# Kernel optimization log

Measured on AMD Instinct MI355X. Metric: run time of the kernel, lower is better.

Reference implementation:

```python
import jax, jax.numpy as jnp
import numpy as np

N, E, F_IN, H, HID, OUT, G, NCLS = 20000, 320000, 128, 4, 64, 128, 64, 10
EPS = 1e-5
NEG_SLOPE = 0.2
# layer specs: (in_dim, heads, out_per_head, concat)
LAYERS = [(F_IN, H, HID, True), (H * HID, H, HID, True), (H * HID, 1, OUT, False)]


def setup_inputs() -> dict:
    key = jax.random.key(0)
    ks = jax.random.split(key, 24)
    s = 0.1
    inp = {
        "x": jax.random.normal(ks[0], (N, F_IN), jnp.float32),
        "edge_index": jax.random.randint(ks[1], (2, E), 0, N, jnp.int32),
        "batch": jnp.sort(jax.random.randint(ks[2], (N,), 0, G, jnp.int32)),
    }
    i = 3
    for li, (din, h, dout, concat) in enumerate(LAYERS):
        inp[f"W{li}"] = jax.random.normal(ks[i], (din, h * dout), jnp.float32) * s; i += 1
        inp[f"asrc{li}"] = jax.random.normal(ks[i], (h, dout), jnp.float32) * s; i += 1
        inp[f"adst{li}"] = jax.random.normal(ks[i], (h, dout), jnp.float32) * s; i += 1
        bdim = h * dout if concat else dout
        inp[f"b{li}"] = jnp.zeros((bdim,), jnp.float32)
        inp[f"gamma{li}"] = jnp.ones((bdim,), jnp.float32)
        inp[f"beta{li}"] = jnp.zeros((bdim,), jnp.float32)
    inp["clf_W"] = jax.random.normal(ks[i], (OUT, NCLS), jnp.float32) * s; i += 1
    inp["clf_b"] = jnp.zeros((NCLS,), jnp.float32)
    inp["dom_W1"] = jax.random.normal(ks[i], (OUT, OUT // 2), jnp.float32) * s; i += 1
    inp["dom_b1"] = jnp.zeros((OUT // 2,), jnp.float32)
    inp["dom_W2"] = jax.random.normal(ks[i], (OUT // 2, 2), jnp.float32) * s; i += 1
    inp["dom_b2"] = jnp.zeros((2,), jnp.float32)
    return inp


def _gat_layer(x, src, dst, W, a_s, a_d, b, heads, dout, concat):
    n = x.shape[0]
    h = (x @ W).reshape(n, heads, dout)                      # [N,H,D]
    es = jnp.sum(h * a_s, axis=-1)                           # [N,H]
    ed = jnp.sum(h * a_d, axis=-1)                           # [N,H]
    e = jax.nn.leaky_relu(es[src] + ed[dst], NEG_SLOPE)      # [E',H]
    m = jax.ops.segment_max(e, dst, num_segments=n)          # segment softmax over dst
    w = jnp.exp(e - m[dst])
    z = jax.ops.segment_sum(w, dst, num_segments=n)
    att = w / z[dst]                                         # [E',H]
    out = jax.ops.segment_sum(h[src] * att[:, :, None], dst, num_segments=n)  # [N,H,D]
    out = out.reshape(n, heads * dout) if concat else out.mean(axis=1)
    return out + b


def _bn(x, gamma, beta):  # training-mode BN forward (batch stats, biased var)
    mu = x.mean(axis=0)
    var = x.var(axis=0)
    return (x - mu) * jax.lax.rsqrt(var + EPS) * gamma + beta


def reference(x, edge_index, batch,
              W0, asrc0, adst0, b0, gamma0, beta0,
              W1, asrc1, adst1, b1, gamma1, beta1,
              W2, asrc2, adst2, b2, gamma2, beta2,
              clf_W, clf_b, dom_W1, dom_b1, dom_W2, dom_b2):
    n = x.shape[0]
    loop = jnp.arange(n, dtype=edge_index.dtype)
    src = jnp.concatenate([edge_index[0], loop])  # add self-loops (PyG default)
    dst = jnp.concatenate([edge_index[1], loop])
    params = [(W0, asrc0, adst0, b0, gamma0, beta0),
              (W1, asrc1, adst1, b1, gamma1, beta1),
              (W2, asrc2, adst2, b2, gamma2, beta2)]
    for (W, a_s, a_d, b, g, be), (_, heads, dout, concat) in zip(params, LAYERS):
        x = _gat_layer(x, src, dst, W, a_s, a_d, b, heads, dout, concat)
        x = jax.nn.relu(_bn(x, g, be))  # dropout disabled (inference)
    counts = jax.ops.segment_sum(jnp.ones((n,), x.dtype), batch, num_segments=G)
    feature = jax.ops.segment_sum(x, batch, num_segments=G) / jnp.maximum(counts, 1.0)[:, None]
    class_output = feature @ clf_W + clf_b
    dom_h = jax.nn.relu(feature @ dom_W1 + dom_b1)  # GRL is identity in forward
    domain_output = dom_h @ dom_W2 + dom_b2
    return (class_output, domain_output, feature)
```

## Files before the change

kernel.cpp:

```cpp
#include <hip/hip_runtime.h>
#include <hip/hip_bf16.h>

#define CAP 64
#define EPSBN 1e-5f
#define NEG_SLOPE 0.2f
#define NPARAM 24
#define POOL_SPLIT 4
#define BNB 256

typedef __attribute__((ext_vector_type(8))) short short8;
typedef __attribute__((ext_vector_type(4))) float f32x4;

static __device__ __forceinline__ float b2f(__hip_bfloat16 v) { return __bfloat162float(v); }
static __device__ __forceinline__ float u2f(unsigned short u) {
    return __uint_as_float(((unsigned int)u) << 16);
}
static __device__ __forceinline__ unsigned short f2b_rne(float f) {
    unsigned int u = __float_as_uint(f);
    u += 0x7FFF + ((u >> 16) & 1);
    return (unsigned short)(u >> 16);
}
static __device__ __forceinline__ bool is_f32(const int* flagcnt) { return *flagcnt > 32; }

__global__ void k_detect(const unsigned short* __restrict__ raw, int* flagcnt) {
    int t = threadIdx.x;
    int c = 0;
    for (int i = t; i < 4096; i += 256) {
        int e = (raw[i] >> 7) & 0xFF;
        if (e >= 200) c++;
    }
    atomicAdd(flagcnt, c);
}

struct CvtTab {
    const void* src[NPARAM];
    float* dst[NPARAM];
    int off[NPARAM + 1];
};

__global__ void k_prep(const void* __restrict__ x_in, unsigned short* __restrict__ xb16,
                       CvtTab tab,
                       unsigned short* __restrict__ Wt0, unsigned short* __restrict__ Wt1,
                       unsigned short* __restrict__ Wt2,
                       const int* flagcnt, int NX, int ptot) {
    bool f32 = is_f32(flagcnt);
    const void* W0r = tab.src[0];
    const void* W1r = tab.src[6];
    const void* W2r = tab.src[12];
    int b0 = NX, b1 = b0 + ptot, b2 = b1 + 256 * 128, b3 = b2 + 256 * 256, b4 = b3 + 128 * 256;
    for (int i = blockIdx.x * blockDim.x + threadIdx.x; i < b4; i += gridDim.x * blockDim.x) {
        if (i < b0) {
            xb16[i] = f32 ? f2b_rne(((const float*)x_in)[i]) : ((const unsigned short*)x_in)[i];
        } else if (i < b1) {
            int ii = i - b0;
            int j = 0;
            while (tab.off[j + 1] <= ii) j++;
            int k = ii - tab.off[j];
            tab.dst[j][k] = f32 ? ((const float*)tab.src[j])[k]
                                : b2f(((const __hip_bfloat16*)tab.src[j])[k]);
        } else if (i < b2) {
            int ii = i - b1;
            int f = ii >> 7, k = ii & 127;
            long src = (long)k * 256 + f;
            Wt0[ii] = f32 ? f2b_rne(((const float*)W0r)[src]) : ((const unsigned short*)W0r)[src];
        } else if (i < b3) {
            int ii = i - b2;
            int f = ii >> 8, k = ii & 255;
            long src = (long)k * 256 + f;
            Wt1[ii] = f32 ? f2b_rne(((const float*)W1r)[src]) : ((const unsigned short*)W1r)[src];
        } else {
            int ii = i - b3;
            int f = ii >> 8, k = ii & 255;
            long src = (long)k * 128 + f;
            Wt2[ii] = f32 ? f2b_rne(((const float*)W2r)[src]) : ((const unsigned short*)W2r)[src];
        }
    }
}

__global__ void k_fill_graph(const int* __restrict__ ei, int* cnt, int* adj, int E) {
    int e = blockIdx.x * blockDim.x + threadIdx.x;
    if (e < E) {
        int s = ei[e];
        int d = ei[E + e];
        int slot = atomicAdd(&cnt[d], 1);
        if (slot < CAP) adj[d * CAP + slot] = s;
    }
}

__global__ __launch_bounds__(256) void k_gemm_mfma(const unsigned short* __restrict__ A,
                                                   const unsigned short* __restrict__ Bt,
                                                   unsigned short* __restrict__ C,
                                                   const float* __restrict__ scale,
                                                   const float* __restrict__ shift,
                                                   int M, int K, int F) {
    __shared__ __align__(16) unsigned short As[64 * 40];
    __shared__ __align__(16) unsigned short Bs[64 * 40];
    int t = threadIdx.x;
    int lane = t & 63, wave = t >> 6;
    int wm = wave & 1, wf = wave >> 1;
    int m0 = blockIdx.x * 64, f0 = blockIdx.y * 64;
    int r = lane & 15, q = lane >> 4;
    int srow = t >> 2, schunk = t & 3;
    f32x4 acc[2][2] = {};
    for (int k0 = 0; k0 < K; k0 += 32) {
        uint4 av = {0, 0, 0, 0};
        int gr = m0 + srow;
        if (gr < M) {
            av = *(const uint4*)(A + (long)gr * K + k0 + schunk * 8);
            if (scale) {
                int fb = k0 + schunk * 8;
                float4 s0 = *(const float4*)(scale + fb);
                float4 s1 = *(const float4*)(scale + fb + 4);
                float4 h0 = *(const float4*)(shift + fb);
                float4 h1 = *(const float4*)(shift + fb + 4);
                unsigned short* ev = (unsigned short*)&av;
                ev[0] = f2b_rne(fmaxf(u2f(ev[0]) * s0.x + h0.x, 0.f));
                ev[1] = f2b_rne(fmaxf(u2f(ev[1]) * s0.y + h0.y, 0.f));
                ev[2] = f2b_rne(fmaxf(u2f(ev[2]) * s0.z + h0.z, 0.f));
                ev[3] = f2b_rne(fmaxf(u2f(ev[3]) * s0.w + h0.w, 0.f));
                ev[4] = f2b_rne(fmaxf(u2f(ev[4]) * s1.x + h1.x, 0.f));
                ev[5] = f2b_rne(fmaxf(u2f(ev[5]) * s1.y + h1.y, 0.f));
                ev[6] = f2b_rne(fmaxf(u2f(ev[6]) * s1.z + h1.z, 0.f));
                ev[7] = f2b_rne(fmaxf(u2f(ev[7]) * s1.w + h1.w, 0.f));
            }
        }
        *(uint4*)&As[srow * 40 + schunk * 8] = av;
        uint4 bv = *(const uint4*)(Bt + (long)(f0 + srow) * K + k0 + schunk * 8);
        *(uint4*)&Bs[srow * 40 + schunk * 8] = bv;
        __syncthreads();
        short8 a0 = *(short8*)&As[(wm * 32 + r) * 40 + q * 8];
        short8 a1 = *(short8*)&As[(wm * 32 + 16 + r) * 40 + q * 8];
        short8 b0 = *(short8*)&Bs[(wf * 32 + r) * 40 + q * 8];
        short8 b1 = *(short8*)&Bs[(wf * 32 + 16 + r) * 40 + q * 8];
        acc[0][0] = __builtin_amdgcn_mfma_f32_16x16x32_bf16(a0, b0, acc[0][0], 0, 0, 0);
        acc[0][1] = __builtin_amdgcn_mfma_f32_16x16x32_bf16(a0, b1, acc[0][1], 0, 0, 0);
        acc[1][0] = __builtin_amdgcn_mfma_f32_16x16x32_bf16(a1, b0, acc[1][0], 0, 0, 0);
        acc[1][1] = __builtin_amdgcn_mfma_f32_16x16x32_bf16(a1, b1, acc[1][1], 0, 0, 0);
        __syncthreads();
    }
    #pragma unroll
    for (int mt = 0; mt < 2; mt++) {
        #pragma unroll
        for (int reg = 0; reg < 4; reg++) {
            int row = m0 + wm * 32 + mt * 16 + q * 4 + reg;
            if (row < M) {
                C[(long)row * F + f0 + wf * 32 + r]      = f2b_rne(acc[mt][0][reg]);
                C[(long)row * F + f0 + wf * 32 + 16 + r] = f2b_rne(acc[mt][1][reg]);
            }
        }
    }
}

template <int F, int H>
__global__ __launch_bounds__(256) void k_agg(const unsigned short* __restrict__ h,
                      const int* __restrict__ cnt, const int* __restrict__ adj,
                      const float* __restrict__ a_s, const float* __restrict__ a_d,
                      const float* __restrict__ bias,
                      unsigned short* __restrict__ out, int n) {
    const int VPL = F / 64;
    const int LPH = 64 / H;
    int lane = threadIdx.x & 63;
    int dst = (blockIdx.x * blockDim.x + threadIdx.x) >> 6;
    if (dst >= n) return;
    float asv[VPL], adv[VPL];
    #pragma unroll
    for (int j = 0; j < VPL; j++) {
        asv[j] = a_s[lane * VPL + j];
        adv[j] = a_d[lane * VPL + j];
    }
    float hs[VPL];
    {
        const unsigned short* hp = h + (long)dst * F + lane * VPL;
        if (VPL == 4) {
            uint2 hv = *(const uint2*)hp;
            hs[0] = __uint_as_float(hv.x << 16); hs[1] = __uint_as_float(hv.x & 0xffff0000u);
            hs[2] = __uint_as_float(hv.y << 16); hs[3] = __uint_as_float(hv.y & 0xffff0000u);
        } else {
            unsigned int hv = *(const unsigned int*)hp;
            hs[0] = __uint_as_float(hv << 16); hs[1] = __uint_as_float(hv & 0xffff0000u);
        }
    }
    float ps = 0.f, pd = 0.f;
    #pragma unroll
    for (int j = 0; j < VPL; j++) { ps += hs[j] * asv[j]; pd += hs[j] * adv[j]; }
    #pragma unroll
    for (int m = 1; m < LPH; m <<= 1) {
        ps += __shfl_xor(ps, m, 64);
        pd += __shfl_xor(pd, m, 64);
    }
    float ed_dst = pd;
    float e = ps + ed_dst;
    e = fmaxf(e, NEG_SLOPE * e);
    float w = __expf(e);
    float z = w;
    float acc[VPL];
    #pragma unroll
    for (int j = 0; j < VPL; j++) acc[j] = w * hs[j];

    int deg = min(cnt[dst], CAP);
    const int* ap = adj + (long)dst * CAP;
    int sl = 0;
    if (deg > 0) sl = ap[lane < deg ? lane : deg - 1];
    for (int base = 0; base < deg; base += 8) {
        float hv[8][VPL];
        #pragma unroll
        for (int c = 0; c < 8; c++) {
            int idx = base + c;
            int ii = idx < deg ? idx : deg - 1;
            int s = __builtin_amdgcn_readlane(sl, ii);
            const unsigned short* hp = h + (long)s * F + lane * VPL;
            if (VPL == 4) {
                uint2 hb = *(const uint2*)hp;
                hv[c][0] = __uint_as_float(hb.x << 16);
                hv[c][1] = __uint_as_float(hb.x & 0xffff0000u);
                hv[c][2] = __uint_as_float(hb.y << 16);
                hv[c][3] = __uint_as_float(hb.y & 0xffff0000u);
            } else {
                unsigned int hb = *(const unsigned int*)hp;
                hv[c][0] = __uint_as_float(hb << 16);
                hv[c][1] = __uint_as_float(hb & 0xffff0000u);
            }
        }
        #pragma unroll
        for (int c = 0; c < 8; c++) {
            float p = 0.f;
            #pragma unroll
            for (int j = 0; j < VPL; j++) p += hv[c][j] * asv[j];
            #pragma unroll
            for (int m = 1; m < LPH; m <<= 1) p += __shfl_xor(p, m, 64);
            float ee = p + ed_dst;
            ee = fmaxf(ee, NEG_SLOPE * ee);
            float ww = __expf(ee);
            if (base + c >= deg) ww = 0.f;
            z += ww;
            #pragma unroll
            for (int j = 0; j < VPL; j++) acc[j] += ww * hv[c][j];
        }
    }
    float invz = 1.f / z;
    unsigned short pk[VPL];
    #pragma unroll
    for (int j = 0; j < VPL; j++)
        pk[j] = f2b_rne(acc[j] * invz + bias[lane * VPL + j]);
    if (VPL == 4) *(ushort4*)(out + (long)dst * F + lane * 4) = *(ushort4*)pk;
    else          *(ushort2*)(out + (long)dst * F + lane * 2) = *(ushort2*)pk;
}

template <int F>
__global__ __launch_bounds__(256) void k_bnpart(const unsigned short* __restrict__ x,
                                                float* __restrict__ partial, int n) {
    const int TPR = F / 8;
    const int RPI = 256 / TPR;
    __shared__ float sm[256 * 17];
    int t = threadIdx.x;
    int fr = t % TPR;
    int rp = t / TPR;
    int f0 = fr * 8;
    float s[8] = {}, q[8] = {};
    for (int r = blockIdx.x * RPI + rp; r < n; r += gridDim.x * RPI) {
        uint4 v = *(const uint4*)(x + (long)r * F + f0);
        const unsigned short* ev = (const unsigned short*)&v;
        #pragma unroll
        for (int j = 0; j < 8; j++) {
            float f = u2f(ev[j]);
            s[j] += f; q[j] += f * f;
        }
    }
    #pragma unroll
    for (int j = 0; j < 8; j++) { sm[t * 17 + j] = s[j]; sm[t * 17 + 8 + j] = q[j]; }
    __syncthreads();
    if (rp == 0) {
        float a[8], b[8];
        #pragma unroll
        for (int j = 0; j < 8; j++) { a[j] = sm[fr * 17 + j]; b[j] = sm[fr * 17 + 8 + j]; }
        for (int p = 1; p < RPI; p++) {
            int o = (p * TPR + fr) * 17;
            #pragma unroll
            for (int j = 0; j < 8; j++) { a[j] += sm[o + j]; b[j] += sm[o + 8 + j]; }
        }
        float* dp = partial + (long)blockIdx.x * 2 * F;
        #pragma unroll
        for (int j = 0; j < 8; j++) { dp[f0 + j] = a[j]; dp[F + f0 + j] = b[j]; }
    }
}

__global__ __launch_bounds__(64) void k_bnfold(const float* __restrict__ partial,
                         const float* __restrict__ gamma, const float* __restrict__ beta,
                         float* __restrict__ scale, float* __restrict__ shift,
                         float invN, int F, int nb) {
    int f = blockIdx.x;
    int l = threadIdx.x;
    float s = 0.f, q = 0.f;
    for (int b = l; b < nb; b += 64) {
        s += partial[(long)b * 2 * F + f];
        q += partial[(long)b * 2 * F + F + f];
    }
    #pragma unroll
    for (int m = 1; m < 64; m <<= 1) {
        s += __shfl_xor(s, m, 64);
        q += __shfl_xor(q, m, 64);
    }
    if (l == 0) {
        float mu = s * invN;
        float var = q * invN - mu * mu;
        float sc = gamma[f] * rsqrtf(var + EPSBN);
        scale[f] = sc;
        shift[f] = beta[f] - mu * sc;
    }
}

static __device__ __forceinline__ int lower_bound_i(const int* __restrict__ a, int n, int v) {
    int lo = 0, hi = n;
    while (lo < hi) { int mid = (lo + hi) >> 1; if (a[mid] < v) lo = mid + 1; else hi = mid; }
    return lo;
}

__global__ __launch_bounds__(256) void k_pool2(const unsigned short* __restrict__ x,
                                               const int* __restrict__ batch,
                                               const float* __restrict__ scale,
                                               const float* __restrict__ shift,
                                               float* __restrict__ featsum,
                                               int* __restrict__ gcnt, int n) {
    const int TPR = 32;
    const int RPI = 8;
    __shared__ float sm[256 * 5];
    int g = blockIdx.x / POOL_SPLIT;
    int part = blockIdx.x % POOL_SPLIT;
    int t = threadIdx.x;
    int fr = t % TPR;
    int rp = t / TPR;
    int f0 = fr * 4;
    int lo = lower_bound_i(batch, n, g);
    int hi = lower_bound_i(batch, n, g + 1);
    float4 sc = *(const float4*)(scale + f0);
    float4 sh = *(const float4*)(shift + f0);
    float a0 = 0.f, a1 = 0.f, a2 = 0.f, a3 = 0.f;
    for (int r = lo + part * RPI + rp; r < hi; r += POOL_SPLIT * RPI) {
        uint2 v = *(const uint2*)(x + (long)r * 128 + f0);
        a0 += fmaxf(u2f((unsigned short)(v.x & 0xffff)) * sc.x + sh.x, 0.f);
        a1 += fmaxf(u2f((unsigned short)(v.x >> 16))    * sc.y + sh.y, 0.f);
        a2 += fmaxf(u2f((unsigned short)(v.y & 0xffff)) * sc.z + sh.z, 0.f);
        a3 += fmaxf(u2f((unsigned short)(v.y >> 16))    * sc.w + sh.w, 0.f);
    }
    sm[t * 5 + 0] = a0; sm[t * 5 + 1] = a1; sm[t * 5 + 2] = a2; sm[t * 5 + 3] = a3;
    __syncthreads();
    if (rp == 0) {
        float b[4];
        #pragma unroll
        for (int j = 0; j < 4; j++) b[j] = sm[fr * 5 + j];
        for (int p = 1; p < RPI; p++)
            #pragma unroll
            for (int j = 0; j < 4; j++) b[j] += sm[(p * TPR + fr) * 5 + j];
        #pragma unroll
        for (int j = 0; j < 4; j++) atomicAdd(&featsum[g * 128 + f0 + j], b[j]);
    }
    if (t == 0 && part == 0) gcnt[g] = hi - lo;
}

__global__ void k_head(const float* __restrict__ featsum, const int* __restrict__ gcnt,
                       const float* __restrict__ clfW, const float* __restrict__ clfb,
                       const float* __restrict__ dW1, const float* __restrict__ db1,
                       const float* __restrict__ dW2, const float* __restrict__ db2,
                       void* __restrict__ out, const int* flagcnt, int G) {
    __shared__ float feat[128];
    __shared__ float dh[64];
    bool f32o = is_f32(flagcnt);
    float* of = (float*)out;
    __hip_bfloat16* ob = (__hip_bfloat16*)out;
    int g = blockIdx.x, t = threadIdx.x;
    float c = fmaxf((float)gcnt[g], 1.f);
    float fv = featsum[g * 128 + t] / c;
    feat[t] = fv;
    int fidx = G * 10 + G * 2 + g * 128 + t;
    if (f32o) of[fidx] = fv; else ob[fidx] = __float2bfloat16(fv);
    __syncthreads();
    if (t < 10) {
        float a = clfb[t];
        for (int k = 0; k < 128; k++) a += feat[k] * clfW[k * 10 + t];
        int idx = g * 10 + t;
        if (f32o) of[idx] = a; else ob[idx] = __float2bfloat16(a);
    }
    if (t < 64) {
        float a = db1[t];
        for (int k = 0; k < 128; k++) a += feat[k] * dW1[k * 64 + t];
        dh[t] = a > 0.f ? a : 0.f;
    }
    __syncthreads();
    if (t < 2) {
        float a = db2[t];
        for (int k = 0; k < 64; k++) a += dh[k] * dW2[k * 2 + t];
        int idx = G * 10 + g * 2 + t;
        if (f32o) of[idx] = a; else ob[idx] = __float2bfloat16(a);
    }
}

extern "C" void kernel_launch(void* const* d_in, const int* in_sizes, int n_in,
                              void* d_out, int out_size, void* d_ws, size_t ws_size,
                              hipStream_t stream) {
    const void* x_in = d_in[0];
    const int* ei    = (const int*)d_in[1];
    const int* batch = (const int*)d_in[2];
    const int N = in_sizes[2];
    const int E = in_sizes[1] / 2;
    const int G = 64;

    char* ws = (char*)d_ws;
    size_t off = 0;
    auto alloc = [&](size_t bytes) {
        void* p = ws + off;
        off += (bytes + 255) & ~(size_t)255;
        return p;
    };

    size_t zstart = off;
    int*   flagcnt   = (int*)alloc(256);
    float* featsum   = (float*)alloc((size_t)G * 128 * 4 + (size_t)G * 4);
    int*   gcnt      = (int*)(featsum + G * 128);
    int*   cnt       = (int*)alloc((size_t)N * 4);
    size_t zbytes = off - zstart;

    int*   adj     = (int*)alloc((size_t)N * CAP * 4);
    unsigned short* xbuf16 = (unsigned short*)alloc((size_t)N * 256 * 2);
    unsigned short* hbuf   = (unsigned short*)alloc((size_t)N * 256 * 2);
    unsigned short* xb16   = (unsigned short*)alloc((size_t)N * 256 * 2);
    unsigned short* Wt0    = (unsigned short*)alloc((size_t)256 * 128 * 2);
    unsigned short* Wt1    = (unsigned short*)alloc((size_t)256 * 256 * 2);
    unsigned short* Wt2    = (unsigned short*)alloc((size_t)128 * 256 * 2);
    float* bnpart  = (float*)alloc((size_t)BNB * 512 * 4);
    float* bnscale = (float*)alloc(3 * 512 * 4);

    float* sc0 = bnscale,        *sh0 = bnscale + 256;
    float* sc1 = bnscale + 512,  *sh1 = bnscale + 768;
    float* sc2 = bnscale + 1024, *sh2 = bnscale + 1280;

    CvtTab tab;
    float* pp[NPARAM];
    int ptot = 0;
    for (int j = 0; j < NPARAM; j++) {
        int cnt_j = in_sizes[3 + j];
        pp[j] = (float*)alloc((size_t)cnt_j * 4);
        tab.src[j] = d_in[3 + j];
        tab.dst[j] = pp[j];
        tab.off[j] = ptot;
        ptot += cnt_j;
    }
    tab.off[NPARAM] = ptot;
    float *asf0 = pp[1], *adf0 = pp[2], *bf0 = pp[3], *gf0 = pp[4], *bef0 = pp[5];
    float *asf1 = pp[7], *adf1 = pp[8], *bf1 = pp[9], *gf1 = pp[10], *bef1 = pp[11];
    float *asf2 = pp[13], *adf2 = pp[14], *bf2 = pp[15], *gf2 = pp[16], *bef2 = pp[17];
    float *clfWf = pp[18], *clfbf = pp[19], *dW1f = pp[20], *db1f = pp[21], *dW2f = pp[22], *db2f = pp[23];

    const int TPB = 256;
    int wgrid = (N + 3) / 4;
    int mblocks = (N + 63) / 64;
    float invN = 1.f / (float)N;

    hipMemsetAsync(ws + zstart, 0, zbytes, stream);
    k_detect<<<1, 256, 0, stream>>>((const unsigned short*)x_in, flagcnt);
    k_prep<<<2048, TPB, 0, stream>>>(x_in, xb16, tab, Wt0, Wt1, Wt2, flagcnt, N * 128, ptot);
    k_fill_graph<<<(E + TPB - 1) / TPB, TPB, 0, stream>>>(ei, cnt, adj, E);

    k_gemm_mfma<<<dim3(mblocks, 4), 256, 0, stream>>>(xb16, Wt0, hbuf, nullptr, nullptr, N, 128, 256);
    k_agg<256, 4><<<wgrid, 256, 0, stream>>>(hbuf, cnt, adj, asf0, adf0, bf0, xbuf16, N);
    k_bnpart<256><<<BNB, 256, 0, stream>>>(xbuf16, bnpart, N);
    k_bnfold<<<256, 64, 0, stream>>>(bnpart, gf0, bef0, sc0, sh0, invN, 256, BNB);

    k_gemm_mfma<<<dim3(mblocks, 4), 256, 0, stream>>>(xbuf16, Wt1, hbuf, sc0, sh0, N, 256, 256);
    k_agg<256, 4><<<wgrid, 256, 0, stream>>>(hbuf, cnt, adj, asf1, adf1, bf1, xbuf16, N);
    k_bnpart<256><<<BNB, 256, 0, stream>>>(xbuf16, bnpart, N);
    k_bnfold<<<256, 64, 0, stream>>>(bnpart, gf1, bef1, sc1, sh1, invN, 256, BNB);

    k_gemm_mfma<<<dim3(mblocks, 2), 256, 0, stream>>>(xbuf16, Wt2, hbuf, sc1, sh1, N, 256, 128);
    k_agg<128, 1><<<wgrid, 256, 0, stream>>>(hbuf, cnt, adj, asf2, adf2, bf2, xbuf16, N);
    k_bnpart<128><<<BNB, 256, 0, stream>>>(xbuf16, bnpart, N);
    k_bnfold<<<128, 64, 0, stream>>>(bnpart, gf2, bef2, sc2, sh2, invN, 128, BNB);

    k_pool2<<<G * POOL_SPLIT, 256, 0, stream>>>(xbuf16, batch, sc2, sh2, featsum, gcnt, N);
    k_head<<<G, 128, 0, stream>>>(featsum, gcnt, clfWf, clfbf, dW1f, db1f, dW2f, db2f,
                                  d_out, flagcnt, G);
}
```

Baseline: 316.3 us.

## Fuse BatchNorm partial statistics into aggregation and enlarge GEMM M-tile

The aggregation kernel now handles 8 destination nodes per wave and accumulates per-feature sum and sum-of-squares of its bf16 outputs. It reduces them across waves in shared memory and writes per-block partials, which removes the separate k_bnpart pass that re-read the full activation buffer. The GEMM tile grows from 64 to 128 rows per block, so each wave issues 8 MFMAs per k-step and each loaded B tile is reused more. LDS padding is also dropped (stride 40 to 32), which may add bank conflicts, and k_bnfold now reduces far more partial blocks (about 625 instead of 256).

Result: slower. 360.6 us (+14.0%).

```diff
diff --git a/kernel.cpp b/kernel.cpp
--- a/kernel.cpp
+++ b/kernel.cpp
@@ -6,7 +6,7 @@
 #define NEG_SLOPE 0.2f
 #define NPARAM 24
 #define POOL_SPLIT 4
-#define BNB 256
+#define DPW 8
 
 typedef __attribute__((ext_vector_type(8))) short short8;
 typedef __attribute__((ext_vector_type(4))) float f32x4;
@@ -93,59 +93,69 @@
                                                    const float* __restrict__ scale,
                                                    const float* __restrict__ shift,
                                                    int M, int K, int F) {
-    __shared__ __align__(16) unsigned short As[64 * 40];
-    __shared__ __align__(16) unsigned short Bs[64 * 40];
+    __shared__ __align__(16) unsigned short As[128 * 32];
+    __shared__ __align__(16) unsigned short Bs[64 * 32];
     int t = threadIdx.x;
     int lane = t & 63, wave = t >> 6;
     int wm = wave & 1, wf = wave >> 1;
-    int m0 = blockIdx.x * 64, f0 = blockIdx.y * 64;
+    int m0 = blockIdx.x * 128, f0 = blockIdx.y * 64;
     int r = lane & 15, q = lane >> 4;
-    int srow = t >> 2, schunk = t & 3;
-    f32x4 acc[2][2] = {};
+    f32x4 acc[4][2] = {};
     for (int k0 = 0; k0 < K; k0 += 32) {
-        uint4 av = {0, 0, 0, 0};
-        int gr = m0 + srow;
-        if (gr < M) {
-            av = *(const uint4*)(A + (long)gr * K + k0 + schunk * 8);
-            if (scale) {
-                int fb = k0 + schunk * 8;
-                float4 s0 = *(const float4*)(scale + fb);
-                float4 s1 = *(const float4*)(scale + fb + 4);
-                float4 h0 = *(const float4*)(shift + fb);
-                float4 h1 = *(const float4*)(shift + fb + 4);
-                unsigned short* ev = (unsigned short*)&av;
-                ev[0] = f2b_rne(fmaxf(u2f(ev[0]) * s0.x + h0.x, 0.f));
-                ev[1] = f2b_rne(fmaxf(u2f(ev[1]) * s0.y + h0.y, 0.f));
-                ev[2] = f2b_rne(fmaxf(u2f(ev[2]) * s0.z + h0.z, 0.f));
-                ev[3] = f2b_rne(fmaxf(u2f(ev[3]) * s0.w + h0.w, 0.f));
-                ev[4] = f2b_rne(fmaxf(u2f(ev[4]) * s1.x + h1.x, 0.f));
-                ev[5] = f2b_rne(fmaxf(u2f(ev[5]) * s1.y + h1.y, 0.f));
-                ev[6] = f2b_rne(fmaxf(u2f(ev[6]) * s1.z + h1.z, 0.f));
-                ev[7] = f2b_rne(fmaxf(u2f(ev[7]) * s1.w + h1.w, 0.f));
+        #pragma unroll
+        for (int i = 0; i < 2; i++) {
+            int c = t + 256 * i;
+            int row = c >> 2, sub = c & 3;
+            int gr = m0 + row;
+            uint4 av = {0, 0, 0, 0};
+            if (gr < M) {
+                av = *(const uint4*)(A + (long)gr * K + k0 + sub * 8);
+                if (scale) {
+                    int fb = k0 + sub * 8;
+                    float4 s0 = *(const float4*)(scale + fb);
+                    float4 s1 = *(const float4*)(scale + fb + 4);
+                    float4 h0 = *(const float4*)(shift + fb);
+                    float4 h1 = *(const float4*)(shift + fb + 4);
+                    unsigned short* ev = (unsigned short*)&av;
+                    ev[0] = f2b_rne(fmaxf(u2f(ev[0]) * s0.x + h0.x, 0.f));
+                    ev[1] = f2b_rne(fmaxf(u2f(ev[1]) * s0.y + h0.y, 0.f));
+                    ev[2] = f2b_rne(fmaxf(u2f(ev[2]) * s0.z + h0.z, 0.f));
+                    ev[3] = f2b_rne(fmaxf(u2f(ev[3]) * s0.w + h0.w, 0.f));
+                    ev[4] = f2b_rne(fmaxf(u2f(ev[4]) * s1.x + h1.x, 0.f));
+                    ev[5] = f2b_rne(fmaxf(u2f(ev[5]) * s1.y + h1.y, 0.f));
+                    ev[6] = f2b_rne(fmaxf(u2f(ev[6]) * s1.z + h1.z, 0.f));
+                    ev[7] = f2b_rne(fmaxf(u2f(ev[7]) * s1.w + h1.w, 0.f));
+                }
             }
-        }
-        *(uint4*)&As[srow * 40 + schunk * 8] = av;
-        uint4 bv = *(const uint4*)(Bt + (long)(f0 + srow) * K + k0 + schunk * 8);
-        *(uint4*)&Bs[srow * 40 + schunk * 8] = bv;
+            *(uint4*)&As[row * 32 + sub * 8] = av;
+        }
+        {
+            int row = t >> 2, sub = t & 3;
+            uint4 bv = *(const uint4*)(Bt + (long)(f0 + row) * K + k0 + sub * 8);
+            *(uint4*)&Bs[row * 32 + sub * 8] = bv;
+        }
         __syncthreads();
-        short8 a0 = *(short8*)&As[(wm * 32 + r) * 40 + q * 8];
-        short8 a1 = *(short8*)&As[(wm * 32 + 16 + r) * 40 + q * 8];
-        short8 b0 = *(short8*)&Bs[(wf * 32 + r) * 40 + q * 8];
-        short8 b1 = *(short8*)&Bs[(wf * 32 + 16 + r) * 40 + q * 8];
-        acc[0][0] = __builtin_amdgcn_mfma_f32_16x16x32_bf16(a0, b0, acc[0][0], 0, 0, 0);
-        acc[0][1] = __builtin_amdgcn_mfma_f32_16x16x32_bf16(a0, b1, acc[0][1], 0, 0, 0);
-        acc[1][0] = __builtin_amdgcn_mfma_f32_16x16x32_bf16(a1, b0, acc[1][0], 0, 0, 0);
-        acc[1][1] = __builtin_amdgcn_mfma_f32_16x16x32_bf16(a1, b1, acc[1][1], 0, 0, 0);
+        short8 a[4], b[2];
+        #pragma unroll
+        for (int i = 0; i < 4; i++) a[i] = *(short8*)&As[(wm * 64 + i * 16 + r) * 32 + q * 8];
+        #pragma unroll
+        for (int j = 0; j < 2; j++) b[j] = *(short8*)&Bs[(wf * 32 + j * 16 + r) * 32 + q * 8];
+        #pragma unroll
+        for (int i = 0; i < 4; i++)
+            #pragma unroll
+            for (int j = 0; j < 2; j++)
+                acc[i][j] = __builtin_amdgcn_mfma_f32_16x16x32_bf16(a[i], b[j], acc[i][j], 0, 0, 0);
         __syncthreads();
     }
     #pragma unroll
-    for (int mt = 0; mt < 2; mt++) {
+    for (int i = 0; i < 4; i++) {
         #pragma unroll
         for (int reg = 0; reg < 4; reg++) {
-            int row = m0 + wm * 32 + mt * 16 + q * 4 + reg;
+            int row = m0 + wm * 64 + i * 16 + q * 4 + reg;
             if (row < M) {
-                C[(long)row * F + f0 + wf * 32 + r]      = f2b_rne(acc[mt][0][reg]);
-                C[(long)row * F + f0 + wf * 32 + 16 + r] = f2b_rne(acc[mt][1][reg]);
+                #pragma unroll
+                for (int j = 0; j < 2; j++)
+                    C[(long)row * F + f0 + wf * 32 + j * 16 + r] = f2b_rne(acc[i][j][reg]);
             }
         }
     }
@@ -156,131 +166,122 @@
                       const int* __restrict__ cnt, const int* __restrict__ adj,
                       const float* __restrict__ a_s, const float* __restrict__ a_d,
                       const float* __restrict__ bias,
-                      unsigned short* __restrict__ out, int n) {
+                      unsigned short* __restrict__ out,
+                      float* __restrict__ partial, int n) {
     const int VPL = F / 64;
     const int LPH = 64 / H;
+    __shared__ float smS[4][F];
+    __shared__ float smQ[4][F];
     int lane = threadIdx.x & 63;
-    int dst = (blockIdx.x * blockDim.x + threadIdx.x) >> 6;
-    if (dst >= n) return;
-    float asv[VPL], adv[VPL];
+    int wave = threadIdx.x >> 6;
+    float asv[VPL], adv[VPL], bsv[VPL];
     #pragma unroll
     for (int j = 0; j < VPL; j++) {
         asv[j] = a_s[lane * VPL + j];
         adv[j] = a_d[lane * VPL + j];
-    }
-    float hs[VPL];
-    {
-        const unsigned short* hp = h + (long)dst * F + lane * VPL;
-        if (VPL == 4) {
-            uint2 hv = *(const uint2*)hp;
-            hs[0] = __uint_as_float(hv.x << 16); hs[1] = __uint_as_float(hv.x & 0xffff0000u);
-            hs[2] = __uint_as_float(hv.y << 16); hs[3] = __uint_as_float(hv.y & 0xffff0000u);
-        } else {
-            unsigned int hv = *(const unsigned int*)hp;
-            hs[0] = __uint_as_float(hv << 16); hs[1] = __uint_as_float(hv & 0xffff0000u);
-        }
-    }
-    float ps = 0.f, pd = 0.f;
+        bsv[j] = bias[lane * VPL + j];
+    }
+    float sacc[VPL] = {}, qacc[VPL] = {};
+    int dst0 = blockIdx.x * 32 + wave * DPW;
+    for (int it = 0; it < DPW; it++) {
+        int dst = dst0 + it;
+        if (dst >= n) break;
+        float hs[VPL];
+        {
+            const unsigned short* hp = h + (long)dst * F + lane * VPL;
+            if (VPL == 4) {
+                uint2 hv = *(const uint2*)hp;
+                hs[0] = __uint_as_float(hv.x << 16); hs[1] = __uint_as_float(hv.x & 0xffff0000u);
+                hs[2] = __uint_as_float(hv.y << 16); hs[3] = __uint_as_float(hv.y & 0xffff0000u);
+            } else {
+                unsigned int hv = *(const unsigned int*)hp;
+                hs[0] = __uint_as_float(hv << 16); hs[1] = __uint_as_float(hv & 0xffff0000u);
+            }
+        }
+        float ps = 0.f, pd = 0.f;
+        #pragma unroll
+        for (int j = 0; j < VPL; j++) { ps += hs[j] * asv[j]; pd += hs[j] * adv[j]; }
+        #pragma unroll
+        for (int m = 1; m < LPH; m <<= 1) {
+            ps += __shfl_xor(ps, m, 64);
+            pd += __shfl_xor(pd, m, 64);
+        }
+        float ed_dst = pd;
+        float e = ps + ed_dst;
+        e = fmaxf(e, NEG_SLOPE * e);
+        float w = __expf(e);
+        float z = w;
+        float acc[VPL];
+        #pragma unroll
+        for (int j = 0; j < VPL; j++) acc[j] = w * hs[j];
+
+        int deg = min(cnt[dst], CAP);
+        const int* ap = adj + (long)dst * CAP;
+        int sl = 0;
+        if (deg > 0) sl = ap[lane < deg ? lane : deg - 1];
+        for (int base = 0; base < deg; base += 8) {
+            float hv[8][VPL];
+            #pragma unroll
+            for (int c = 0; c < 8; c++) {
+                int idx = base + c;
+                int ii = idx < deg ? idx : deg - 1;
+                int s = __builtin_amdgcn_readlane(sl, ii);
+                const unsigned short* hp = h + (long)s * F + lane * VPL;
+                if (VPL == 4) {
+                    uint2 hb = *(const uint2*)hp;
+                    hv[c][0] = __uint_as_float(hb.x << 16);
+                    hv[c][1] = __uint_as_float(hb.x & 0xffff0000u);
+                    hv[c][2] = __uint_as_float(hb.y << 16);
+                    hv[c][3] = __uint_as_float(hb.y & 0xffff0000u);
+                } else {
+                    unsigned int hb = *(const unsigned int*)hp;
+                    hv[c][0] = __uint_as_float(hb << 16);
+                    hv[c][1] = __uint_as_float(hb & 0xffff0000u);
+                }
+            }
+            #pragma unroll
+            for (int c = 0; c < 8; c++) {
+                float p = 0.f;
+                #pragma unroll
+                for (int j = 0; j < VPL; j++) p += hv[c][j] * asv[j];
+                #pragma unroll
+                for (int m = 1; m < LPH; m <<= 1) p += __shfl_xor(p, m, 64);
+                float ee = p + ed_dst;
+                ee = fmaxf(ee, NEG_SLOPE * ee);
+                float ww = __expf(ee);
+                if (base + c >= deg) ww = 0.f;
+                z += ww;
+                #pragma unroll
+                for (int j = 0; j < VPL; j++) acc[j] += ww * hv[c][j];
+            }
+        }
+        float invz = 1.f / z;
+        unsigned short pk[VPL];
+        #pragma unroll
+        for (int j = 0; j < VPL; j++) {
+            pk[j] = f2b_rne(acc[j] * invz + bsv[j]);
+            float vr = u2f(pk[j]);
+            sacc[j] += vr;
+            qacc[j] += vr * vr;
+        }
+        if (VPL == 4) *(ushort4*)(out + (long)dst * F + lane * 4) = *(ushort4*)pk;
+        else          *(ushort2*)(out + (long)dst * F + lane * 2) = *(ushort2*)pk;
+    }
     #pragma unroll
-    for (int j = 0; j < VPL; j++) { ps += hs[j] * asv[j]; pd += hs[j] * adv[j]; }
-    #pragma unroll
-    for (int m = 1; m < LPH; m <<= 1) {
-        ps += __shfl_xor(ps, m, 64);
-        pd += __shfl_xor(pd, m, 64);
-    }
-    float ed_dst = pd;
-    float e = ps + ed_dst;
-    e = fmaxf(e, NEG_SLOPE * e);
-    float w = __expf(e);
-    float z = w;
-    float acc[VPL];
-    #pragma unroll
-    for (int j = 0; j < VPL; j++) acc[j] = w * hs[j];
-
-    int deg = min(cnt[dst], CAP);
-    const int* ap = adj + (long)dst * CAP;
-    int sl = 0;
-    if (deg > 0) sl = ap[lane < deg ? lane : deg - 1];
-    for (int base = 0; base < deg; base += 8) {
-        float hv[8][VPL];
-        #pragma unroll
-        for (int c = 0; c < 8; c++) {
-            int idx = base + c;
-            int ii = idx < deg ? idx : deg - 1;
-            int s = __builtin_amdgcn_readlane(sl, ii);
-            const unsigned short* hp = h + (long)s * F + lane * VPL;
-            if (VPL == 4) {
-                uint2 hb = *(const uint2*)hp;
-                hv[c][0] = __uint_as_float(hb.x << 16);
-                hv[c][1] = __uint_as_float(hb.x & 0xffff0000u);
-                hv[c][2] = __uint_as_float(hb.y << 16);
-                hv[c][3] = __uint_as_float(hb.y & 0xffff0000u);
-            } else {
-                unsigned int hb = *(const unsigned int*)hp;
-                hv[c][0] = __uint_as_float(hb << 16);
-                hv[c][1] = __uint_as_float(hb & 0xffff0000u);
-            }
-        }
-        #pragma unroll
-        for (int c = 0; c < 8; c++) {
-            float p = 0.f;
-            #pragma unroll
-            for (int j = 0; j < VPL; j++) p += hv[c][j] * asv[j];
-            #pragma unroll
-            for (int m = 1; m < LPH; m <<= 1) p += __shfl_xor(p, m, 64);
-            float ee = p + ed_dst;
-            ee = fmaxf(ee, NEG_SLOPE * ee);
-            float ww = __expf(ee);
-            if (base + c >= deg) ww = 0.f;
-            z += ww;
-            #pragma unroll
-            for (int j = 0; j < VPL; j++) acc[j] += ww * hv[c][j];
-        }
-    }
-    float invz = 1.f / z;
-    unsigned short pk[VPL];
-    #pragma unroll
-    for (int j = 0; j < VPL; j++)
-        pk[j] = f2b_rne(acc[j] * invz + bias[lane * VPL + j]);
-    if (VPL == 4) *(ushort4*)(out + (long)dst * F + lane * 4) = *(ushort4*)pk;
-    else          *(ushort2*)(out + (long)dst * F + lane * 2) = *(ushort2*)pk;
-}
-
-template <int F>
-__global__ __launch_bounds__(256) void k_bnpart(const unsigned short* __restrict__ x,
-                                                float* __restrict__ partial, int n) {
-    const int TPR = F / 8;
-    const int RPI = 256 / TPR;
-    __shared__ float sm[256 * 17];
-    int t = threadIdx.x;
-    int fr = t % TPR;
-    int rp = t / TPR;
-    int f0 = fr * 8;
-    float s[8] = {}, q[8] = {};
-    for (int r = blockIdx.x * RPI + rp; r < n; r += gridDim.x * RPI) {
-        uint4 v = *(const uint4*)(x + (long)r * F + f0);
-        const unsigned short* ev = (const unsigned short*)&v;
-        #pragma unroll
-        for (int j = 0; j < 8; j++) {
-            float f = u2f(ev[j]);
-            s[j] += f; q[j] += f * f;
-        }
-    }
-    #pragma unroll
-    for (int j = 0; j < 8; j++) { sm[t * 17 + j] = s[j]; sm[t * 17 + 8 + j] = q[j]; }
+    for (int j = 0; j < VPL; j++) {
+        smS[wave][lane * VPL + j] = sacc[j];
+        smQ[wave][lane * VPL + j] = qacc[j];
+    }
     __syncthreads();
-    if (rp == 0) {
-        float a[8], b[8];
-        #pragma unroll
-        for (int j = 0; j < 8; j++) { a[j] = sm[fr * 17 + j]; b[j] = sm[fr * 17 + 8 + j]; }
-        for (int p = 1; p < RPI; p++) {
-            int o = (p * TPR + fr) * 17;
-            #pragma unroll
-            for (int j = 0; j < 8; j++) { a[j] += sm[o + j]; b[j] += sm[o + 8 + j]; }
-        }
-        float* dp = partial + (long)blockIdx.x * 2 * F;
-        #pragma unroll
-        for (int j = 0; j < 8; j++) { dp[f0 + j] = a[j]; dp[F + f0 + j] = b[j]; }
+    if (wave == 0) {
+        #pragma unroll
+        for (int j = 0; j < VPL; j++) {
+            int f = lane * VPL + j;
+            float s = smS[0][f] + smS[1][f] + smS[2][f] + smS[3][f];
+            float q = smQ[0][f] + smQ[1][f] + smQ[2][f] + smQ[3][f];
+            partial[(long)blockIdx.x * 2 * F + f] = s;
+            partial[(long)blockIdx.x * 2 * F + F + f] = q;
+        }
     }
 }
 
@@ -412,6 +413,8 @@
         return p;
     };
 
+    int ablocks = (N + 31) / 32;
+
     size_t zstart = off;
     int*   flagcnt   = (int*)alloc(256);
     float* featsum   = (float*)alloc((size_t)G * 128 * 4 + (size_t)G * 4);
@@ -426,7 +429,7 @@
     unsigned short* Wt0    = (unsigned short*)alloc((size_t)256 * 128 * 2);
     unsigned short* Wt1    = (unsigned short*)alloc((size_t)256 * 256 * 2);
     unsigned short* Wt2    = (unsigned short*)alloc((size_t)128 * 256 * 2);
-    float* bnpart  = (float*)alloc((size_t)BNB * 512 * 4);
+    float* bnpart  = (float*)alloc((size_t)ablocks * 512 * 4);
     float* bnscale = (float*)alloc(3 * 512 * 4);
 
     float* sc0 = bnscale,        *sh0 = bnscale + 256;
@@ -451,8 +454,7 @@
     float *clfWf = pp[18], *clfbf = pp[19], *dW1f = pp[20], *db1f = pp[21], *dW2f = pp[22], *db2f = pp[23];
 
     const int TPB = 256;
-    int wgrid = (N + 3) / 4;
-    int mblocks = (N + 63) / 64;
+    int mblocks = (N + 127) / 128;
     float invN = 1.f / (float)N;
 
     hipMemsetAsync(ws + zstart, 0, zbytes, stream);
@@ -461,19 +463,16 @@
     k_fill_graph<<<(E + TPB - 1) / TPB, TPB, 0, stream>>>(ei, cnt, adj, E);
 
     k_gemm_mfma<<<dim3(mblocks, 4), 256, 0, stream>>>(xb16, Wt0, hbuf, nullptr, nullptr, N, 128, 256);
-    k_agg<256, 4><<<wgrid, 256, 0, stream>>>(hbuf, cnt, adj, asf0, adf0, bf0, xbuf16, N);
-    k_bnpart<256><<<BNB, 256, 0, stream>>>(xbuf16, bnpart, N);
-    k_bnfold<<<256, 64, 0, stream>>>(bnpart, gf0, bef0, sc0, sh0, invN, 256, BNB);
+    k_agg<256, 4><<<ablocks, 256, 0, stream>>>(hbuf, cnt, adj, asf0, adf0, bf0, xbuf16, bnpart, N);
+    k_bnfold<<<256, 64, 0, stream>>>(bnpart, gf0, bef0, sc0, sh0, invN, 256, ablocks);
 
     k_gemm_mfma<<<dim3(mblocks, 4), 256, 0, stream>>>(xbuf16, Wt1, hbuf, sc0, sh0, N, 256, 256);
-    k_agg<256, 4><<<wgrid, 256, 0, stream>>>(hbuf, cnt, adj, asf1, adf1, bf1, xbuf16, N);
-    k_bnpart<256><<<BNB, 256, 0, stream>>>(xbuf16, bnpart, N);
-    k_bnfold<<<256, 64, 0, stream>>>(bnpart, gf1, bef1, sc1, sh1, invN, 256, BNB);
+    k_agg<256, 4><<<ablocks, 256, 0, stream>>>(hbuf, cnt, adj, asf1, adf1, bf1, xbuf16, bnpart, N);
+    k_bnfold<<<256, 64, 0, stream>>>(bnpart, gf1, bef1, sc1, sh1, invN, 256, ablocks);
 
     k_gemm_mfma<<<dim3(mblocks, 2), 256, 0, stream>>>(xbuf16, Wt2, hbuf, sc1, sh1, N, 256, 128);
-    k_agg<128, 1><<<wgrid, 256, 0, stream>>>(hbuf, cnt, adj, asf2, adf2, bf2, xbuf16, N);
-    k_bnpart<128><<<BNB, 256, 0, stream>>>(xbuf16, bnpart, N);
-    k_bnfold<<<128, 64, 0, stream>>>(bnpart, gf2, bef2, sc2, sh2, invN, 128, BNB);
+    k_agg<128, 1><<<ablocks, 256, 0, stream>>>(hbuf, cnt, adj, asf2, adf2, bf2, xbuf16, bnpart, N);
+    k_bnfold<<<128, 64, 0, stream>>>(bnpart, gf2, bef2, sc2, sh2, invN, 128, ablocks);
 
     k_pool2<<<G * POOL_SPLIT, 256, 0, stream>>>(xbuf16, batch, sc2, sh2, featsum, gcnt, N);
     k_head<<<G, 128, 0, stream>>>(featsum, gcnt, clfWf, clfbf, dW1f, db1f, dW2f, db2f,
```
